# Kernel tuning notes

Measured on AMD Instinct MI355X. Metric: run time of the kernel, lower is better.

Reference implementation:

```python
import jax, jax.numpy as jnp
import numpy as np

N_NODES = 40000
N_EDGES = 640000
F_IN = 128
HID = 128
N_CLASSES = 10
N_GRAPHS = 64


def _gcn_conv(x, row, col, norm, W, b, n_nodes):
    h = x @ W                                   # [N, H]
    msg = h[row] * norm[:, None]                # [E+N, H] gather + scale
    out = jax.ops.segment_sum(msg, col, num_segments=n_nodes)  # scatter-add
    return out + b


def setup_inputs() -> dict:
    key = jax.random.key(0)
    ks = jax.random.split(key, 8)
    x = jax.random.normal(ks[0], (N_NODES, F_IN), dtype=jnp.float32)
    edge_index = jax.random.randint(ks[1], (2, N_EDGES), 0, N_NODES, dtype=jnp.int32)
    batch = jnp.sort(jax.random.randint(ks[2], (N_NODES,), 0, N_GRAPHS, dtype=jnp.int32))
    s1 = 1.0 / np.sqrt(F_IN)
    s2 = 1.0 / np.sqrt(HID)
    W1 = jax.random.normal(ks[3], (F_IN, HID), dtype=jnp.float32) * s1
    W2 = jax.random.normal(ks[4], (HID, HID), dtype=jnp.float32) * s2
    W3 = jax.random.normal(ks[5], (HID, HID), dtype=jnp.float32) * s2
    Wl = jax.random.normal(ks[6], (HID, N_CLASSES), dtype=jnp.float32) * s2
    b1 = jnp.zeros((HID,), jnp.float32)
    b2 = jnp.zeros((HID,), jnp.float32)
    b3 = jnp.zeros((HID,), jnp.float32)
    bl = jnp.zeros((N_CLASSES,), jnp.float32)
    return {"x": x, "edge_index": edge_index, "batch": batch,
            "W1": W1, "b1": b1, "W2": W2, "b2": b2, "W3": W3, "b3": b3,
            "Wl": Wl, "bl": bl}


def reference(x, edge_index, batch, W1, b1, W2, b2, W3, b3, Wl, bl):
    n = x.shape[0]
    # add self-loops (PyG add_remaining_self_loops with weight 1)
    loops = jnp.arange(n, dtype=edge_index.dtype)
    row = jnp.concatenate([edge_index[0], loops])
    col = jnp.concatenate([edge_index[1], loops])
    w = jnp.ones(row.shape, dtype=x.dtype)
    # symmetric normalization: deg over target nodes incl. self-loops
    deg = jax.ops.segment_sum(w, col, num_segments=n)
    dis = jnp.where(deg > 0, jax.lax.rsqrt(deg), 0.0)
    norm = dis[row] * dis[col]                  # [E+N]

    h = jax.nn.relu(_gcn_conv(x, row, col, norm, W1, b1, n))
    h = jax.nn.relu(_gcn_conv(h, row, col, norm, W2, b2, n))
    h = jax.nn.relu(_gcn_conv(h, row, col, norm, W3, b3, n))

    # global mean pool over graph ids
    sums = jax.ops.segment_sum(h, batch, num_segments=N_GRAPHS)      # [G, H]
    cnts = jax.ops.segment_sum(jnp.ones((n,), h.dtype), batch, num_segments=N_GRAPHS)
    pooled = sums / jnp.maximum(cnts, 1.0)[:, None]
    # dropout(p=0.2) is identity in eval mode
    return pooled @ Wl + bl                     # [G, num_classes]
```

## Files before the change

kernel.cpp:

```cpp
#include <hip/hip_runtime.h>
#include <hip/hip_bf16.h>

#define N_NODES   40000
#define N_EDGES   640000
#define F         128
#define N_GRAPHS  64
#define N_CLASSES 10

typedef short bf16x8 __attribute__((ext_vector_type(8)));
typedef float f32x4  __attribute__((ext_vector_type(4)));

__device__ __forceinline__ unsigned short f2bf(float f) {
    union { float f; unsigned u; } v; v.f = f;
    unsigned r = v.u + 0x7fffu + ((v.u >> 16) & 1u);
    return (unsigned short)(r >> 16);
}
__device__ __forceinline__ float bflo(unsigned u) { return __uint_as_float(u << 16); }
__device__ __forceinline__ float bfhi(unsigned u) { return __uint_as_float(u & 0xffff0000u); }
__device__ __forceinline__ unsigned pack2(float a, float b) {
    return (unsigned)f2bf(a) | ((unsigned)f2bf(b) << 16);
}

__global__ void wcvt_kernel(const float* __restrict__ W1, const float* __restrict__ W2,
                            const float* __restrict__ W3, unsigned short* __restrict__ Wt) {
    int idx = blockIdx.x * 256 + threadIdx.x;
    int l = idx >> 14;
    int r = idx & 16383;
    int c = r >> 7, k = r & 127;
    const float* W = (l == 0) ? W1 : ((l == 1) ? W2 : W3);
    Wt[idx] = f2bf(W[k * 128 + c]);
}

__global__ __launch_bounds__(1024) void scan_kernel(
    const int* __restrict__ deg, int* __restrict__ rowptr,
    int* __restrict__ cursor, float* __restrict__ dis) {
    __shared__ int wsum[16];
    __shared__ int tile_total_s;
    const int tid  = threadIdx.x;
    const int lane = tid & 63;
    const int wave = tid >> 6;
    int running = 0;

    for (int t = 0; t < 10; ++t) {
        const int base = t * 4096 + tid * 4;
        int4 d = make_int4(0, 0, 0, 0);
        if (base < N_NODES) d = *(const int4*)(deg + base);
        const int sown = d.x + d.y + d.z + d.w;

        int s = sown;
#pragma unroll
        for (int off = 1; off < 64; off <<= 1) {
            int n = __shfl_up(s, off, 64);
            if (lane >= off) s += n;
        }
        if (lane == 63) wsum[wave] = s;
        __syncthreads();

        if (wave == 0) {
            int v = (lane < 16) ? wsum[lane] : 0;
#pragma unroll
            for (int off = 1; off < 16; off <<= 1) {
                int n = __shfl_up(v, off, 64);
                if (lane >= off) v += n;
            }
            if (lane < 16) wsum[lane] = v;
            if (lane == 15) tile_total_s = v;
        }
        __syncthreads();

        int excl = running + (wave ? wsum[wave - 1] : 0) + (s - sown);
        if (base < N_NODES) {
            int4 r;
            r.x = excl;
            r.y = r.x + d.x;
            r.z = r.y + d.y;
            r.w = r.z + d.z;
            *(int4*)(rowptr + base) = r;
            *(int4*)(cursor + base) = r;
            float4 di;
            di.x = rsqrtf((float)d.x + 1.0f);
            di.y = rsqrtf((float)d.y + 1.0f);
            di.z = rsqrtf((float)d.z + 1.0f);
            di.w = rsqrtf((float)d.w + 1.0f);
            *(float4*)(dis + base) = di;
        }
        running += tile_total_s;
        __syncthreads();
    }
}

__global__ void fill_kernel(const int* __restrict__ row, const int* __restrict__ col,
                            int* __restrict__ cursor, int* __restrict__ csr_src) {
    int e = blockIdx.x * 256 + threadIdx.x;
    if (e < N_EDGES) {
        int pos = atomicAdd(&cursor[col[e]], 1);
        csr_src[pos] = row[e];
    }
}

#define APITCH 136
template<bool ABF16, bool RELU, bool SCALE, bool COUNT>
__global__ __launch_bounds__(256) void gemm_mfma(
    const void* __restrict__ Araw, const unsigned short* __restrict__ Wt,
    const float* __restrict__ bias, const float* __restrict__ dis,
    unsigned short* __restrict__ Hb,
    const int* __restrict__ cnt_col, int* __restrict__ cnt_deg) {
    __shared__ unsigned short As[64 * APITCH];
    __shared__ unsigned short Ws[128 * APITCH];
    const int tid  = threadIdx.x;
    const int row0 = blockIdx.x * 64;

    if (COUNT) {
        int t = (blockIdx.x * 256 + tid) * 4;
#pragma unroll
        for (int j = 0; j < 4; ++j) atomicAdd(&cnt_deg[cnt_col[t + j]], 1);
    }

    {
        const uint4* src = (const uint4*)Wt;
#pragma unroll
        for (int j = 0; j < 8; ++j) {
            int c4 = tid + j * 256;
            int c  = c4 >> 4;
            int o  = c4 & 15;
            *(uint4*)(Ws + c * APITCH + o * 8) = src[c4];
        }
    }
    if (ABF16) {
        const uint4* src = (const uint4*)Araw;
#pragma unroll
        for (int j = 0; j < 4; ++j) {
            int c4 = tid + j * 256;
            int r  = c4 >> 4;
            int p  = c4 & 15;
            int o  = p << 3;
            uint4 hv = src[(size_t)(row0 + r) * 16 + p];
            float f0 = bflo(hv.x), f1 = bfhi(hv.x), f2 = bflo(hv.y), f3 = bfhi(hv.y);
            float f4_ = bflo(hv.z), f5 = bfhi(hv.z), f6 = bflo(hv.w), f7 = bfhi(hv.w);
            if (bias) {
                float4 b0 = *(const float4*)(bias + o);
                float4 b1 = *(const float4*)(bias + o + 4);
                f0 += b0.x; f1 += b0.y; f2 += b0.z; f3 += b0.w;
                f4_ += b1.x; f5 += b1.y; f6 += b1.z; f7 += b1.w;
            }
            if (RELU) {
                f0 = fmaxf(f0, 0.f); f1 = fmaxf(f1, 0.f); f2 = fmaxf(f2, 0.f);
                f3 = fmaxf(f3, 0.f); f4_ = fmaxf(f4_, 0.f); f5 = fmaxf(f5, 0.f);
                f6 = fmaxf(f6, 0.f); f7 = fmaxf(f7, 0.f);
            }
            uint4 pk;
            pk.x = pack2(f0, f1); pk.y = pack2(f2, f3);
            pk.z = pack2(f4_, f5); pk.w = pack2(f6, f7);
            *(uint4*)(As + r * APITCH + o) = pk;
        }
    } else {
        const float* A = (const float*)Araw;
#pragma unroll
        for (int j = 0; j < 8; ++j) {
            int c4 = tid + j * 256;
            int r  = c4 >> 5;
            int o  = (c4 & 31) << 2;
            float4 v = *(const float4*)(A + (size_t)(row0 + r) * F + o);
            if (bias) {
                v.x += bias[o + 0]; v.y += bias[o + 1];
                v.z += bias[o + 2]; v.w += bias[o + 3];
            }
            if (RELU) {
                v.x = fmaxf(v.x, 0.f); v.y = fmaxf(v.y, 0.f);
                v.z = fmaxf(v.z, 0.f); v.w = fmaxf(v.w, 0.f);
            }
            uint2 p;
            p.x = pack2(v.x, v.y);
            p.y = pack2(v.z, v.w);
            *(uint2*)(As + r * APITCH + o) = p;
        }
    }
    __syncthreads();

    const int lane = tid & 63;
    const int wave = tid >> 6;
    const int m16  = lane & 15;
    const int quad = lane >> 4;

    f32x4 acc[8];
#pragma unroll
    for (int t = 0; t < 8; ++t) acc[t] = (f32x4)(0.0f);

#pragma unroll
    for (int ks = 0; ks < 128; ks += 32) {
        bf16x8 a = *(const bf16x8*)(As + (wave * 16 + m16) * APITCH + ks + quad * 8);
#pragma unroll
        for (int t = 0; t < 8; ++t) {
            bf16x8 b = *(const bf16x8*)(Ws + (t * 16 + m16) * APITCH + ks + quad * 8);
            acc[t] = __builtin_amdgcn_mfma_f32_16x16x32_bf16(a, b, acc[t], 0, 0, 0);
        }
    }

    const int rbase = row0 + wave * 16 + quad * 4;
    float sc[4];
#pragma unroll
    for (int rg = 0; rg < 4; ++rg) sc[rg] = SCALE ? dis[rbase + rg] : 1.0f;
#pragma unroll
    for (int t = 0; t < 8; ++t) {
        int col = t * 16 + m16;
#pragma unroll
        for (int rg = 0; rg < 4; ++rg)
            Hb[(size_t)(rbase + rg) * F + col] = f2bf(acc[t][rg] * sc[rg]);
    }
}

template <bool SCALED>
__global__ __launch_bounds__(256) void gather_kernel(
    const unsigned short* __restrict__ Hb, const int* __restrict__ csr_src,
    const int* __restrict__ rowptr, const int* __restrict__ deg,
    const float* __restrict__ dis, unsigned short* __restrict__ AGGb) {
    const int gid  = blockIdx.x * 256 + threadIdx.x;
    const int v    = gid >> 6;
    if (v >= N_NODES) return;
    const int lane = threadIdx.x & 63;
    const int part = lane & 15;
    const int quad = lane >> 4;

    const int start = rowptr[v];
    const int len   = deg[v];
    const uint4* Hp = (const uint4*)Hb + part;

    float acc[8];
#pragma unroll
    for (int i = 0; i < 8; ++i) acc[i] = 0.f;

    for (int j0 = 0; j0 < len; j0 += 64) {
        int m = len - j0; if (m > 64) m = 64;
        int nidx = (lane < m) ? csr_src[start + j0 + lane] : 0;
        for (int j = 0; j < m; j += 16) {
            int   r[4];
            float w[4];
            uint4 h[4];
#pragma unroll
            for (int u = 0; u < 4; ++u) {
                int  sl    = j + u * 4 + quad;
                bool valid = sl < m;
                r[u] = __shfl(nidx, valid ? sl : 0, 64);
                w[u] = valid ? (SCALED ? dis[r[u]] : 1.0f) : 0.0f;
            }
#pragma unroll
            for (int u = 0; u < 4; ++u) h[u] = Hp[(size_t)r[u] * 16];
#pragma unroll
            for (int u = 0; u < 4; ++u) {
                acc[0] = fmaf(bflo(h[u].x), w[u], acc[0]);
                acc[1] = fmaf(bfhi(h[u].x), w[u], acc[1]);
                acc[2] = fmaf(bflo(h[u].y), w[u], acc[2]);
                acc[3] = fmaf(bfhi(h[u].y), w[u], acc[3]);
                acc[4] = fmaf(bflo(h[u].z), w[u], acc[4]);
                acc[5] = fmaf(bfhi(h[u].z), w[u], acc[5]);
                acc[6] = fmaf(bflo(h[u].w), w[u], acc[6]);
                acc[7] = fmaf(bfhi(h[u].w), w[u], acc[7]);
            }
        }
    }

#pragma unroll
    for (int i = 0; i < 8; ++i) {
        acc[i] += __shfl_xor(acc[i], 16, 64);
        acc[i] += __shfl_xor(acc[i], 32, 64);
    }

    if (quad == 0) {
        float dc  = dis[v];
        float ws_ = SCALED ? dc : 1.0f;
        uint4 h = Hp[(size_t)v * 16];
        acc[0] = fmaf(bflo(h.x), ws_, acc[0]); acc[1] = fmaf(bfhi(h.x), ws_, acc[1]);
        acc[2] = fmaf(bflo(h.y), ws_, acc[2]); acc[3] = fmaf(bfhi(h.y), ws_, acc[3]);
        acc[4] = fmaf(bflo(h.z), ws_, acc[4]); acc[5] = fmaf(bfhi(h.z), ws_, acc[5]);
        acc[6] = fmaf(bflo(h.w), ws_, acc[6]); acc[7] = fmaf(bfhi(h.w), ws_, acc[7]);
        uint4 pk;
        pk.x = pack2(acc[0] * dc, acc[1] * dc);
        pk.y = pack2(acc[2] * dc, acc[3] * dc);
        pk.z = pack2(acc[4] * dc, acc[5] * dc);
        pk.w = pack2(acc[6] * dc, acc[7] * dc);
        *((uint4*)AGGb + (size_t)v * 16 + part) = pk;
    }
}

#define POOL_NODES 100
__global__ __launch_bounds__(256) void pool_kernel(
    const unsigned short* __restrict__ AGGb, const int* __restrict__ batch,
    const float* __restrict__ b3,
    float* __restrict__ pooled, float* __restrict__ cnt) {
    const int tid  = threadIdx.x;
    const int f4   = (tid & 31) << 2;
    const int slot = tid >> 5;
    const int base = blockIdx.x * POOL_NODES;
    const float4 bf = *(const float4*)(b3 + f4);

    float4 acc = make_float4(0.f, 0.f, 0.f, 0.f);
    float c = 0.f;
    int gcur = -1;
    for (int j = slot; j < POOL_NODES; j += 8) {
        int v = base + j;
        int g = batch[v];
        if (g != gcur) {
            if (gcur >= 0) {
                float* dst = pooled + gcur * F + f4;
                atomicAdd(dst + 0, acc.x); atomicAdd(dst + 1, acc.y);
                atomicAdd(dst + 2, acc.z); atomicAdd(dst + 3, acc.w);
                if (f4 == 0) atomicAdd(&cnt[gcur], c);
            }
            acc = make_float4(0.f, 0.f, 0.f, 0.f); c = 0.f; gcur = g;
        }
        uint2 a = *(const uint2*)(AGGb + (size_t)v * F + f4);
        acc.x += fmaxf(bflo(a.x) + bf.x, 0.f);
        acc.y += fmaxf(bfhi(a.x) + bf.y, 0.f);
        acc.z += fmaxf(bflo(a.y) + bf.z, 0.f);
        acc.w += fmaxf(bfhi(a.y) + bf.w, 0.f);
        c += 1.f;
    }
    if (gcur >= 0) {
        float* dst = pooled + gcur * F + f4;
        atomicAdd(dst + 0, acc.x); atomicAdd(dst + 1, acc.y);
        atomicAdd(dst + 2, acc.z); atomicAdd(dst + 3, acc.w);
        if (f4 == 0) atomicAdd(&cnt[gcur], c);
    }
}

__global__ void head_kernel(const float* __restrict__ pooled,
                            const float* __restrict__ cnt,
                            const float* __restrict__ Wl,
                            const float* __restrict__ bl,
                            float* __restrict__ out) {
    int tid = threadIdx.x;
    if (tid >= N_GRAPHS * N_CLASSES) return;
    int g = tid / N_CLASSES, c = tid % N_CLASSES;
    float acc = 0.f;
    for (int ff = 0; ff < F; ++ff)
        acc += pooled[g * F + ff] * Wl[ff * N_CLASSES + c];
    out[g * N_CLASSES + c] = acc / fmaxf(cnt[g], 1.f) + bl[c];
}

extern "C" void kernel_launch(void* const* d_in, const int* in_sizes, int n_in,
                              void* d_out, int out_size, void* d_ws, size_t ws_size,
                              hipStream_t stream) {
    const float* x    = (const float*)d_in[0];
    const int*   ei   = (const int*)d_in[1];
    const int*   bat  = (const int*)d_in[2];
    const float* W1   = (const float*)d_in[3];
    const float* b1   = (const float*)d_in[4];
    const float* W2   = (const float*)d_in[5];
    const float* b2   = (const float*)d_in[6];
    const float* W3   = (const float*)d_in[7];
    const float* b3   = (const float*)d_in[8];
    const float* Wl   = (const float*)d_in[9];
    const float* bl   = (const float*)d_in[10];
    float* out = (float*)d_out;

    const int* row = ei;
    const int* col = ei + N_EDGES;

    float*          ws      = (float*)d_ws;
    float*          dis     = ws;
    unsigned short* Hb      = (unsigned short*)(dis + N_NODES);
    unsigned short* AGGb    = Hb + (size_t)N_NODES * F;
    float*          pooled  = (float*)(AGGb + (size_t)N_NODES * F);
    float*          cnt     = pooled + N_GRAPHS * F;
    int*            deg     = (int*)(cnt + N_GRAPHS);
    int*            rowptr  = deg + N_NODES;
    int*            cursor  = rowptr + N_NODES;
    int*            csr_src = cursor + N_NODES;
    unsigned short* Wtb     = (unsigned short*)(csr_src + N_EDGES);

    const int edgeGrid   = (N_EDGES + 255) / 256;
    const int gemmGrid   = N_NODES / 64;
    const int gatherGrid = (N_NODES * 64) / 256;

    hipMemsetAsync(deg, 0, N_NODES * sizeof(int), stream);
    wcvt_kernel<<<192, 256, 0, stream>>>(W1, W2, W3, Wtb);

    gemm_mfma<false, false, false, true><<<gemmGrid, 256, 0, stream>>>(
        x, Wtb, nullptr, nullptr, Hb, col, deg);
    scan_kernel<<<1, 1024, 0, stream>>>(deg, rowptr, cursor, dis);
    fill_kernel<<<edgeGrid, 256, 0, stream>>>(row, col, cursor, csr_src);
    gather_kernel<true><<<gatherGrid, 256, 0, stream>>>(Hb, csr_src, rowptr, deg, dis, AGGb);

    gemm_mfma<true, true, true, false><<<gemmGrid, 256, 0, stream>>>(
        AGGb, Wtb + 16384, b1, dis, Hb, nullptr, nullptr);
    gather_kernel<false><<<gatherGrid, 256, 0, stream>>>(Hb, csr_src, rowptr, deg, dis, AGGb);

    gemm_mfma<true, true, true, false><<<gemmGrid, 256, 0, stream>>>(
        AGGb, Wtb + 32768, b2, dis, Hb, nullptr, nullptr);
    gather_kernel<false><<<gatherGrid, 256, 0, stream>>>(Hb, csr_src, rowptr, deg, dis, AGGb);

    hipMemsetAsync(pooled, 0, (N_GRAPHS * F + N_GRAPHS) * sizeof(float), stream);
    pool_kernel<<<N_NODES / POOL_NODES, 256, 0, stream>>>(AGGb, bat, b3, pooled, cnt);
    head_kernel<<<1, N_GRAPHS * N_CLASSES, 0, stream>>>(pooled, cnt, Wl, bl, out);
}
```

Measured before the change: 304.8 us.

## Fuse neighbor aggregation into next-layer GEMM and final pooling

Each GCN aggregation (CSR gather) is folded into the following GEMM kernel: every block gathers its 64 destination rows straight into shared memory, applies bias, scale and ReLU, then runs the MFMA product. The last aggregation is merged with global mean pooling, so the aggregated bf16 rows are never written to or re-read from global memory, and three kernel launches go away. The cost is much less parallelism in the gather stage: 625 blocks, each with 4 waves walking 16 nodes serially, replace 10000 blocks with one wave per node. That can hide memory latency poorly and leave the block idle before its GEMM starts.

```diff
diff --git a/kernel.cpp b/kernel.cpp
--- a/kernel.cpp
+++ b/kernel.cpp
@@ -20,6 +20,8 @@
 __device__ __forceinline__ unsigned pack2(float a, float b) {
     return (unsigned)f2bf(a) | ((unsigned)f2bf(b) << 16);
 }
+
+#define APITCH 136
 
 __global__ void wcvt_kernel(const float* __restrict__ W1, const float* __restrict__ W2,
                             const float* __restrict__ W3, unsigned short* __restrict__ Wt) {
@@ -98,134 +100,14 @@
     }
 }
 
-#define APITCH 136
-template<bool ABF16, bool RELU, bool SCALE, bool COUNT>
-__global__ __launch_bounds__(256) void gemm_mfma(
-    const void* __restrict__ Araw, const unsigned short* __restrict__ Wt,
-    const float* __restrict__ bias, const float* __restrict__ dis,
-    unsigned short* __restrict__ Hb,
-    const int* __restrict__ cnt_col, int* __restrict__ cnt_deg) {
-    __shared__ unsigned short As[64 * APITCH];
-    __shared__ unsigned short Ws[128 * APITCH];
-    const int tid  = threadIdx.x;
-    const int row0 = blockIdx.x * 64;
-
-    if (COUNT) {
-        int t = (blockIdx.x * 256 + tid) * 4;
-#pragma unroll
-        for (int j = 0; j < 4; ++j) atomicAdd(&cnt_deg[cnt_col[t + j]], 1);
-    }
-
-    {
-        const uint4* src = (const uint4*)Wt;
-#pragma unroll
-        for (int j = 0; j < 8; ++j) {
-            int c4 = tid + j * 256;
-            int c  = c4 >> 4;
-            int o  = c4 & 15;
-            *(uint4*)(Ws + c * APITCH + o * 8) = src[c4];
-        }
-    }
-    if (ABF16) {
-        const uint4* src = (const uint4*)Araw;
-#pragma unroll
-        for (int j = 0; j < 4; ++j) {
-            int c4 = tid + j * 256;
-            int r  = c4 >> 4;
-            int p  = c4 & 15;
-            int o  = p << 3;
-            uint4 hv = src[(size_t)(row0 + r) * 16 + p];
-            float f0 = bflo(hv.x), f1 = bfhi(hv.x), f2 = bflo(hv.y), f3 = bfhi(hv.y);
-            float f4_ = bflo(hv.z), f5 = bfhi(hv.z), f6 = bflo(hv.w), f7 = bfhi(hv.w);
-            if (bias) {
-                float4 b0 = *(const float4*)(bias + o);
-                float4 b1 = *(const float4*)(bias + o + 4);
-                f0 += b0.x; f1 += b0.y; f2 += b0.z; f3 += b0.w;
-                f4_ += b1.x; f5 += b1.y; f6 += b1.z; f7 += b1.w;
-            }
-            if (RELU) {
-                f0 = fmaxf(f0, 0.f); f1 = fmaxf(f1, 0.f); f2 = fmaxf(f2, 0.f);
-                f3 = fmaxf(f3, 0.f); f4_ = fmaxf(f4_, 0.f); f5 = fmaxf(f5, 0.f);
-                f6 = fmaxf(f6, 0.f); f7 = fmaxf(f7, 0.f);
-            }
-            uint4 pk;
-            pk.x = pack2(f0, f1); pk.y = pack2(f2, f3);
-            pk.z = pack2(f4_, f5); pk.w = pack2(f6, f7);
-            *(uint4*)(As + r * APITCH + o) = pk;
-        }
-    } else {
-        const float* A = (const float*)Araw;
-#pragma unroll
-        for (int j = 0; j < 8; ++j) {
-            int c4 = tid + j * 256;
-            int r  = c4 >> 5;
-            int o  = (c4 & 31) << 2;
-            float4 v = *(const float4*)(A + (size_t)(row0 + r) * F + o);
-            if (bias) {
-                v.x += bias[o + 0]; v.y += bias[o + 1];
-                v.z += bias[o + 2]; v.w += bias[o + 3];
-            }
-            if (RELU) {
-                v.x = fmaxf(v.x, 0.f); v.y = fmaxf(v.y, 0.f);
-                v.z = fmaxf(v.z, 0.f); v.w = fmaxf(v.w, 0.f);
-            }
-            uint2 p;
-            p.x = pack2(v.x, v.y);
-            p.y = pack2(v.z, v.w);
-            *(uint2*)(As + r * APITCH + o) = p;
-        }
-    }
-    __syncthreads();
-
-    const int lane = tid & 63;
-    const int wave = tid >> 6;
-    const int m16  = lane & 15;
-    const int quad = lane >> 4;
-
-    f32x4 acc[8];
-#pragma unroll
-    for (int t = 0; t < 8; ++t) acc[t] = (f32x4)(0.0f);
-
-#pragma unroll
-    for (int ks = 0; ks < 128; ks += 32) {
-        bf16x8 a = *(const bf16x8*)(As + (wave * 16 + m16) * APITCH + ks + quad * 8);
-#pragma unroll
-        for (int t = 0; t < 8; ++t) {
-            bf16x8 b = *(const bf16x8*)(Ws + (t * 16 + m16) * APITCH + ks + quad * 8);
-            acc[t] = __builtin_amdgcn_mfma_f32_16x16x32_bf16(a, b, acc[t], 0, 0, 0);
-        }
-    }
-
-    const int rbase = row0 + wave * 16 + quad * 4;
-    float sc[4];
-#pragma unroll
-    for (int rg = 0; rg < 4; ++rg) sc[rg] = SCALE ? dis[rbase + rg] : 1.0f;
-#pragma unroll
-    for (int t = 0; t < 8; ++t) {
-        int col = t * 16 + m16;
-#pragma unroll
-        for (int rg = 0; rg < 4; ++rg)
-            Hb[(size_t)(rbase + rg) * F + col] = f2bf(acc[t][rg] * sc[rg]);
-    }
-}
-
 template <bool SCALED>
-__global__ __launch_bounds__(256) void gather_kernel(
-    const unsigned short* __restrict__ Hb, const int* __restrict__ csr_src,
+__device__ __forceinline__ void gather_node(
+    int v, const uint4* __restrict__ Hp, const int* __restrict__ csr_src,
     const int* __restrict__ rowptr, const int* __restrict__ deg,
-    const float* __restrict__ dis, unsigned short* __restrict__ AGGb) {
-    const int gid  = blockIdx.x * 256 + threadIdx.x;
-    const int v    = gid >> 6;
-    if (v >= N_NODES) return;
-    const int lane = threadIdx.x & 63;
-    const int part = lane & 15;
-    const int quad = lane >> 4;
-
+    const float* __restrict__ dis, int lane, int part, int quad,
+    float acc[8]) {
     const int start = rowptr[v];
     const int len   = deg[v];
-    const uint4* Hp = (const uint4*)Hb + part;
-
-    float acc[8];
 #pragma unroll
     for (int i = 0; i < 8; ++i) acc[i] = 0.f;
 
@@ -258,68 +140,231 @@
             }
         }
     }
-
 #pragma unroll
     for (int i = 0; i < 8; ++i) {
         acc[i] += __shfl_xor(acc[i], 16, 64);
         acc[i] += __shfl_xor(acc[i], 32, 64);
     }
-
-    if (quad == 0) {
-        float dc  = dis[v];
-        float ws_ = SCALED ? dc : 1.0f;
-        uint4 h = Hp[(size_t)v * 16];
-        acc[0] = fmaf(bflo(h.x), ws_, acc[0]); acc[1] = fmaf(bfhi(h.x), ws_, acc[1]);
-        acc[2] = fmaf(bflo(h.y), ws_, acc[2]); acc[3] = fmaf(bfhi(h.y), ws_, acc[3]);
-        acc[4] = fmaf(bflo(h.z), ws_, acc[4]); acc[5] = fmaf(bfhi(h.z), ws_, acc[5]);
-        acc[6] = fmaf(bflo(h.w), ws_, acc[6]); acc[7] = fmaf(bfhi(h.w), ws_, acc[7]);
-        uint4 pk;
-        pk.x = pack2(acc[0] * dc, acc[1] * dc);
-        pk.y = pack2(acc[2] * dc, acc[3] * dc);
-        pk.z = pack2(acc[4] * dc, acc[5] * dc);
-        pk.w = pack2(acc[6] * dc, acc[7] * dc);
-        *((uint4*)AGGb + (size_t)v * 16 + part) = pk;
-    }
-}
-
-#define POOL_NODES 100
-__global__ __launch_bounds__(256) void pool_kernel(
-    const unsigned short* __restrict__ AGGb, const int* __restrict__ batch,
+}
+
+__global__ __launch_bounds__(256) void gemm1_kernel(
+    const float* __restrict__ A, const unsigned short* __restrict__ Wt,
+    unsigned short* __restrict__ Hb,
+    const int* __restrict__ cnt_col, int* __restrict__ cnt_deg) {
+    __shared__ unsigned short As[64 * APITCH];
+    __shared__ unsigned short Ws[128 * APITCH];
+    const int tid  = threadIdx.x;
+    const int row0 = blockIdx.x * 64;
+
+    {
+        int t = (blockIdx.x * 256 + tid) * 4;
+#pragma unroll
+        for (int j = 0; j < 4; ++j) atomicAdd(&cnt_deg[cnt_col[t + j]], 1);
+    }
+
+    {
+        const uint4* src = (const uint4*)Wt;
+#pragma unroll
+        for (int j = 0; j < 8; ++j) {
+            int c4 = tid + j * 256;
+            int c  = c4 >> 4;
+            int o  = c4 & 15;
+            *(uint4*)(Ws + c * APITCH + o * 8) = src[c4];
+        }
+    }
+#pragma unroll
+    for (int j = 0; j < 8; ++j) {
+        int c4 = tid + j * 256;
+        int r  = c4 >> 5;
+        int o  = (c4 & 31) << 2;
+        float4 v = *(const float4*)(A + (size_t)(row0 + r) * F + o);
+        uint2 p;
+        p.x = pack2(v.x, v.y);
+        p.y = pack2(v.z, v.w);
+        *(uint2*)(As + r * APITCH + o) = p;
+    }
+    __syncthreads();
+
+    const int lane = tid & 63;
+    const int wave = tid >> 6;
+    const int m16  = lane & 15;
+    const int quad = lane >> 4;
+
+    f32x4 acc[8];
+#pragma unroll
+    for (int t = 0; t < 8; ++t) acc[t] = (f32x4)(0.0f);
+
+#pragma unroll
+    for (int ks = 0; ks < 128; ks += 32) {
+        bf16x8 a = *(const bf16x8*)(As + (wave * 16 + m16) * APITCH + ks + quad * 8);
+#pragma unroll
+        for (int t = 0; t < 8; ++t) {
+            bf16x8 b = *(const bf16x8*)(Ws + (t * 16 + m16) * APITCH + ks + quad * 8);
+            acc[t] = __builtin_amdgcn_mfma_f32_16x16x32_bf16(a, b, acc[t], 0, 0, 0);
+        }
+    }
+
+    const int rbase = row0 + wave * 16 + quad * 4;
+#pragma unroll
+    for (int t = 0; t < 8; ++t) {
+        int col = t * 16 + m16;
+#pragma unroll
+        for (int rg = 0; rg < 4; ++rg)
+            Hb[(size_t)(rbase + rg) * F + col] = f2bf(acc[t][rg]);
+    }
+}
+
+template <bool SCALED>
+__global__ __launch_bounds__(256) void fused_agg_gemm(
+    const unsigned short* __restrict__ Hb_in, const unsigned short* __restrict__ Wt,
+    const float* __restrict__ bias, const float* __restrict__ dis,
+    const int* __restrict__ csr_src, const int* __restrict__ rowptr,
+    const int* __restrict__ deg, unsigned short* __restrict__ Hb_out) {
+    __shared__ unsigned short As[64 * APITCH];
+    __shared__ unsigned short Ws[128 * APITCH];
+    const int tid  = threadIdx.x;
+    const int row0 = blockIdx.x * 64;
+    const int lane = tid & 63;
+    const int wave = tid >> 6;
+    const int part = lane & 15;
+    const int quad = lane >> 4;
+
+    {
+        const uint4* src = (const uint4*)Wt;
+#pragma unroll
+        for (int j = 0; j < 8; ++j) {
+            int c4 = tid + j * 256;
+            int c  = c4 >> 4;
+            int o  = c4 & 15;
+            *(uint4*)(Ws + c * APITCH + o * 8) = src[c4];
+        }
+    }
+
+    const uint4* Hp = (const uint4*)Hb_in + part;
+    for (int i = 0; i < 16; ++i) {
+        const int v = row0 + wave * 16 + i;
+        float acc[8];
+        gather_node<SCALED>(v, Hp, csr_src, rowptr, deg, dis, lane, part, quad, acc);
+        if (quad == 0) {
+            const float dc  = dis[v];
+            const float ws_ = SCALED ? dc : 1.0f;
+            uint4 h = Hp[(size_t)v * 16];
+            acc[0] = fmaf(bflo(h.x), ws_, acc[0]); acc[1] = fmaf(bfhi(h.x), ws_, acc[1]);
+            acc[2] = fmaf(bflo(h.y), ws_, acc[2]); acc[3] = fmaf(bfhi(h.y), ws_, acc[3]);
+            acc[4] = fmaf(bflo(h.z), ws_, acc[4]); acc[5] = fmaf(bfhi(h.z), ws_, acc[5]);
+            acc[6] = fmaf(bflo(h.w), ws_, acc[6]); acc[7] = fmaf(bfhi(h.w), ws_, acc[7]);
+            const int o = part << 3;
+            float4 b0 = *(const float4*)(bias + o);
+            float4 b1 = *(const float4*)(bias + o + 4);
+            float f0 = fmaxf(fmaf(acc[0], dc, b0.x), 0.f);
+            float f1 = fmaxf(fmaf(acc[1], dc, b0.y), 0.f);
+            float f2 = fmaxf(fmaf(acc[2], dc, b0.z), 0.f);
+            float f3 = fmaxf(fmaf(acc[3], dc, b0.w), 0.f);
+            float f4_ = fmaxf(fmaf(acc[4], dc, b1.x), 0.f);
+            float f5 = fmaxf(fmaf(acc[5], dc, b1.y), 0.f);
+            float f6 = fmaxf(fmaf(acc[6], dc, b1.z), 0.f);
+            float f7 = fmaxf(fmaf(acc[7], dc, b1.w), 0.f);
+            uint4 pk;
+            pk.x = pack2(f0, f1); pk.y = pack2(f2, f3);
+            pk.z = pack2(f4_, f5); pk.w = pack2(f6, f7);
+            *(uint4*)(As + (wave * 16 + i) * APITCH + o) = pk;
+        }
+    }
+    __syncthreads();
+
+    const int m16 = lane & 15;
+    f32x4 acc[8];
+#pragma unroll
+    for (int t = 0; t < 8; ++t) acc[t] = (f32x4)(0.0f);
+
+#pragma unroll
+    for (int ks = 0; ks < 128; ks += 32) {
+        bf16x8 a = *(const bf16x8*)(As + (wave * 16 + m16) * APITCH + ks + quad * 8);
+#pragma unroll
+        for (int t = 0; t < 8; ++t) {
+            bf16x8 b = *(const bf16x8*)(Ws + (t * 16 + m16) * APITCH + ks + quad * 8);
+            acc[t] = __builtin_amdgcn_mfma_f32_16x16x32_bf16(a, b, acc[t], 0, 0, 0);
+        }
+    }
+
+    const int rbase = row0 + wave * 16 + quad * 4;
+    float sc[4];
+#pragma unroll
+    for (int rg = 0; rg < 4; ++rg) sc[rg] = dis[rbase + rg];
+#pragma unroll
+    for (int t = 0; t < 8; ++t) {
+        int col = t * 16 + m16;
+#pragma unroll
+        for (int rg = 0; rg < 4; ++rg)
+            Hb_out[(size_t)(rbase + rg) * F + col] = f2bf(acc[t][rg] * sc[rg]);
+    }
+}
+
+#define PNODES 40
+__global__ __launch_bounds__(256) void pool_gather_kernel(
+    const unsigned short* __restrict__ Hb, const int* __restrict__ csr_src,
+    const int* __restrict__ rowptr, const int* __restrict__ deg,
+    const float* __restrict__ dis, const int* __restrict__ batch,
     const float* __restrict__ b3,
     float* __restrict__ pooled, float* __restrict__ cnt) {
     const int tid  = threadIdx.x;
-    const int f4   = (tid & 31) << 2;
-    const int slot = tid >> 5;
-    const int base = blockIdx.x * POOL_NODES;
-    const float4 bf = *(const float4*)(b3 + f4);
-
-    float4 acc = make_float4(0.f, 0.f, 0.f, 0.f);
+    const int lane = tid & 63;
+    const int wave = tid >> 6;
+    const int part = lane & 15;
+    const int quad = lane >> 4;
+    const int base = blockIdx.x * PNODES;
+    const uint4* Hp = (const uint4*)Hb + part;
+    const int o = part << 3;
+
+    float4 bb0 = *(const float4*)(b3 + o);
+    float4 bb1 = *(const float4*)(b3 + o + 4);
+
+    float pacc[8];
+#pragma unroll
+    for (int i = 0; i < 8; ++i) pacc[i] = 0.f;
     float c = 0.f;
     int gcur = -1;
-    for (int j = slot; j < POOL_NODES; j += 8) {
-        int v = base + j;
-        int g = batch[v];
-        if (g != gcur) {
-            if (gcur >= 0) {
-                float* dst = pooled + gcur * F + f4;
-                atomicAdd(dst + 0, acc.x); atomicAdd(dst + 1, acc.y);
-                atomicAdd(dst + 2, acc.z); atomicAdd(dst + 3, acc.w);
-                if (f4 == 0) atomicAdd(&cnt[gcur], c);
+
+    for (int j = wave; j < PNODES; j += 4) {
+        const int v = base + j;
+        const int g = batch[v];
+        float acc[8];
+        gather_node<false>(v, Hp, csr_src, rowptr, deg, dis, lane, part, quad, acc);
+        if (quad == 0) {
+            if (g != gcur) {
+                if (gcur >= 0) {
+                    float* dst = pooled + gcur * F + o;
+#pragma unroll
+                    for (int i = 0; i < 8; ++i) atomicAdd(dst + i, pacc[i]);
+                    if (part == 0) atomicAdd(&cnt[gcur], c);
+                }
+#pragma unroll
+                for (int i = 0; i < 8; ++i) pacc[i] = 0.f;
+                c = 0.f;
             }
-            acc = make_float4(0.f, 0.f, 0.f, 0.f); c = 0.f; gcur = g;
-        }
-        uint2 a = *(const uint2*)(AGGb + (size_t)v * F + f4);
-        acc.x += fmaxf(bflo(a.x) + bf.x, 0.f);
-        acc.y += fmaxf(bfhi(a.x) + bf.y, 0.f);
-        acc.z += fmaxf(bflo(a.y) + bf.z, 0.f);
-        acc.w += fmaxf(bfhi(a.y) + bf.w, 0.f);
-        c += 1.f;
-    }
-    if (gcur >= 0) {
-        float* dst = pooled + gcur * F + f4;
-        atomicAdd(dst + 0, acc.x); atomicAdd(dst + 1, acc.y);
-        atomicAdd(dst + 2, acc.z); atomicAdd(dst + 3, acc.w);
-        if (f4 == 0) atomicAdd(&cnt[gcur], c);
+            const float dc = dis[v];
+            uint4 h = Hp[(size_t)v * 16];
+            acc[0] += bflo(h.x); acc[1] += bfhi(h.x);
+            acc[2] += bflo(h.y); acc[3] += bfhi(h.y);
+            acc[4] += bflo(h.z); acc[5] += bfhi(h.z);
+            acc[6] += bflo(h.w); acc[7] += bfhi(h.w);
+            pacc[0] += fmaxf(fmaf(acc[0], dc, bb0.x), 0.f);
+            pacc[1] += fmaxf(fmaf(acc[1], dc, bb0.y), 0.f);
+            pacc[2] += fmaxf(fmaf(acc[2], dc, bb0.z), 0.f);
+            pacc[3] += fmaxf(fmaf(acc[3], dc, bb0.w), 0.f);
+            pacc[4] += fmaxf(fmaf(acc[4], dc, bb1.x), 0.f);
+            pacc[5] += fmaxf(fmaf(acc[5], dc, bb1.y), 0.f);
+            pacc[6] += fmaxf(fmaf(acc[6], dc, bb1.z), 0.f);
+            pacc[7] += fmaxf(fmaf(acc[7], dc, bb1.w), 0.f);
+            c += 1.f;
+        }
+        gcur = g;
+    }
+    if (quad == 0 && gcur >= 0) {
+        float* dst = pooled + gcur * F + o;
+#pragma unroll
+        for (int i = 0; i < 8; ++i) atomicAdd(dst + i, pacc[i]);
+        if (part == 0) atomicAdd(&cnt[gcur], c);
     }
 }
 
@@ -358,9 +403,9 @@
 
     float*          ws      = (float*)d_ws;
     float*          dis     = ws;
-    unsigned short* Hb      = (unsigned short*)(dis + N_NODES);
-    unsigned short* AGGb    = Hb + (size_t)N_NODES * F;
-    float*          pooled  = (float*)(AGGb + (size_t)N_NODES * F);
+    unsigned short* Hb1     = (unsigned short*)(dis + N_NODES);
+    unsigned short* Hb2     = Hb1 + (size_t)N_NODES * F;
+    float*          pooled  = (float*)(Hb2 + (size_t)N_NODES * F);
     float*          cnt     = pooled + N_GRAPHS * F;
     int*            deg     = (int*)(cnt + N_GRAPHS);
     int*            rowptr  = deg + N_NODES;
@@ -368,28 +413,24 @@
     int*            csr_src = cursor + N_NODES;
     unsigned short* Wtb     = (unsigned short*)(csr_src + N_EDGES);
 
-    const int edgeGrid   = (N_EDGES + 255) / 256;
-    const int gemmGrid   = N_NODES / 64;
-    const int gatherGrid = (N_NODES * 64) / 256;
+    const int edgeGrid = (N_EDGES + 255) / 256;
+    const int gemmGrid = N_NODES / 64;
 
     hipMemsetAsync(deg, 0, N_NODES * sizeof(int), stream);
+    hipMemsetAsync(pooled, 0, (N_GRAPHS * F + N_GRAPHS) * sizeof(float), stream);
     wcvt_kernel<<<192, 256, 0, stream>>>(W1, W2, W3, Wtb);
 
-    gemm_mfma<false, false, false, true><<<gemmGrid, 256, 0, stream>>>(
-        x, Wtb, nullptr, nullptr, Hb, col, deg);
+    gemm1_kernel<<<gemmGrid, 256, 0, stream>>>(x, Wtb, Hb1, col, deg);
     scan_kernel<<<1, 1024, 0, stream>>>(deg, rowptr, cursor, dis);
     fill_kernel<<<edgeGrid, 256, 0, stream>>>(row, col, cursor, csr_src);
-    gather_kernel<true><<<gatherGrid, 256, 0, stream>>>(Hb, csr_src, rowptr, deg, dis, AGGb);
-
-    gemm_mfma<true, true, true, false><<<gemmGrid, 256, 0, stream>>>(
-        AGGb, Wtb + 16384, b1, dis, Hb, nullptr, nullptr);
-    gather_kernel<false><<<gatherGrid, 256, 0, stream>>>(Hb, csr_src, rowptr, deg, dis, AGGb);
-
-    gemm_mfma<true, true, true, false><<<gemmGrid, 256, 0, stream>>>(
-        AGGb, Wtb + 32768, b2, dis, Hb, nullptr, nullptr);
-    gather_kernel<false><<<gatherGrid, 256, 0, stream>>>(Hb, csr_src, rowptr, deg, dis, AGGb);
-
-    hipMemsetAsync(pooled, 0, (N_GRAPHS * F + N_GRAPHS) * sizeof(float), stream);
-    pool_kernel<<<N_NODES / POOL_NODES, 256, 0, stream>>>(AGGb, bat, b3, pooled, cnt);
+
+    fused_agg_gemm<true><<<gemmGrid, 256, 0, stream>>>(
+        Hb1, Wtb + 16384, b1, dis, csr_src, rowptr, deg, Hb2);
+
+    fused_agg_gemm<false><<<gemmGrid, 256, 0, stream>>>(
+        Hb2, Wtb + 32768, b2, dis, csr_src, rowptr, deg, Hb1);
+
+    pool_gather_kernel<<<N_NODES / PNODES, 256, 0, stream>>>(
+        Hb1, csr_src, rowptr, deg, dis, bat, b3, pooled, cnt);
     head_kernel<<<1, N_GRAPHS * N_CLASSES, 0, stream>>>(pooled, cnt, Wl, bl, out);
 }
```

Result: slower. 324.7 us (+6.5%).
